# Kernel tuning notes

Measured on AMD Instinct MI355X. Metric: run time of the kernel, lower is better.

## Reference

```python
import jax, jax.numpy as jnp
import numpy as np

K = 10  # value-iteration steps


def _conv(x, w):
    # NCHW x OIHW -> NCHW, stride 1, SAME padding (pad=2 for 5x5, pad=0 for 1x1)
    return jax.lax.conv_general_dilated(
        x, w, window_strides=(1, 1), padding='SAME',
        dimension_numbers=('NCHW', 'OIHW', 'NCHW'))


def setup_inputs() -> dict:
    key = jax.random.key(0)
    ks = jax.random.split(key, 6)
    B, H, W = 64, 64, 64
    dim_h, n_hat, n_act = 150, 8, 4
    maze = jax.random.randint(ks[0], (B, H, W), 0, 3)
    # fixed embedding table from the torch module
    emb = jnp.array([[0.0, 0.0], [1.0, 0.0], [0.0, 10.0]], dtype=jnp.float32)
    encode_w = jax.random.normal(ks[1], (dim_h, 2, 5, 5), dtype=jnp.float32) * 0.05
    encode_b = jnp.zeros((dim_h,), dtype=jnp.float32)
    r_w = jax.random.normal(ks[2], (1, dim_h, 1, 1), dtype=jnp.float32) * 0.05
    q_w = jax.random.normal(ks[3], (n_hat, 1, 5, 5), dtype=jnp.float32) * 0.05
    # torch inits self.w to zeros; use small randn so the recurrence is non-trivial
    w = jax.random.normal(ks[4], (n_hat, 1, 5, 5), dtype=jnp.float32) * 0.05
    fc_w = jax.random.normal(ks[5], (n_act, n_hat), dtype=jnp.float32) * 0.1
    return dict(maze=maze, emb=emb, encode_w=encode_w, encode_b=encode_b,
                r_w=r_w, q_w=q_w, w=w, fc_w=fc_w)


def reference(maze, emb, encode_w, encode_b, r_w, q_w, w, fc_w):
    # embed: [B,H,W] -> [B,H,W,2] -> [B,2,H,W]
    m = emb[maze].transpose(0, 3, 1, 2)
    h = _conv(m, encode_w) + encode_b[None, :, None, None]  # [B,150,H,W]
    r = _conv(h, r_w)                                        # [B,1,H,W]
    q = _conv(r, q_w)                                        # [B,8,H,W]
    wk = jnp.concatenate([q_w, w], axis=1)                   # [8,2,5,5]

    def step(q, _):
        v = jnp.max(q, axis=1, keepdims=True)                # [B,1,H,W]
        q = _conv(jnp.concatenate([r, v], axis=1), wk)       # [B,8,H,W]
        return q, None

    q, _ = jax.lax.scan(step, q, None, length=K)
    q = q.transpose(0, 2, 3, 1)                              # [B,H,W,8]
    return q @ fc_w.T                                        # [B,H,W,4]
```

## Files before the change

kernel.cpp:

```cpp
#include <hip/hip_runtime.h>
#include <hip/hip_bf16.h>


#define NHAT 8
#define DIMH 150
#define VI_WAVES 12

typedef float v2f __attribute__((ext_vector_type(2)));

__global__ __launch_bounds__(512) void rq_kernel(
    const int* __restrict__ maze, const float* __restrict__ emb,
    const float* __restrict__ encode_w, const float* __restrict__ encode_b,
    const float* __restrict__ r_w, const float* __restrict__ q_w,
    float* __restrict__ q0g) {
  __shared__ float wpart[5][50];
  __shared__ float bpart[152];
  __shared__ float weff[2][25];
  __shared__ float Ts[4][25];
  __shared__ float bsh;
  __shared__ v2f qw2[25][4];
  __shared__ unsigned char mzt[24][68];
  __shared__ float rt[20][68];

  int tid = threadIdx.x;
  int b = blockIdx.y, A0 = blockIdx.x * 16;

  if (tid < 100) {
    int k = tid >> 2, j = tid & 3;
    qw2[k][j] = (v2f){q_w[(2 * j) * 25 + k], q_w[(2 * j + 1) * 25 + k]};
  }
  if (tid >= 256 && tid < 506) {
    int t2 = tid - 256;
    int chunk = t2 / 50, ik = t2 % 50;
    int i = ik / 25, k = ik % 25;
    int c0 = chunk * 30;
    float s = 0.f;
    for (int c = c0; c < c0 + 30; ++c)
      s += r_w[c] * encode_w[c * 50 + i * 25 + k];
    wpart[chunk][ik] = s;
  }
  if (tid >= 100 && tid < 250) {
    int c = tid - 100;
    bpart[c] = r_w[c] * encode_b[c];
  }
  for (int i = tid; i < 24 * 68; i += 512) {
    int mr = i / 68, mc = i % 68;
    int gy = A0 - 4 + mr, gx = mc - 2;
    unsigned char v = 3;
    if (gy >= 0 && gy < 64 && gx >= 0 && gx < 64)
      v = (unsigned char)maze[(b * 64 + gy) * 64 + gx];
    mzt[mr][mc] = v;
  }
  __syncthreads();
  if (tid < 50) {
    float s = 0.f;
#pragma unroll
    for (int ch = 0; ch < 5; ++ch) s += wpart[ch][tid];
    weff[tid / 25][tid % 25] = s;
  }
  if (tid == 50) {
    float s = 0.f;
    for (int c = 0; c < 150; ++c) s += bpart[c];
    bsh = s;
  }
  __syncthreads();
  if (tid < 100) {
    int val = tid / 25, k = tid % 25;
    float t = 0.f;
    if (val < 3) t = weff[0][k] * emb[val * 2] + weff[1][k] * emb[val * 2 + 1];
    Ts[val][k] = t;
  }
  __syncthreads();
  for (int i = tid; i < 20 * 68; i += 512) {
    int rr = i / 68, cc = i % 68;
    int gy = A0 - 2 + rr, gx = cc - 2;
    float v = 0.f;
    if (gy >= 0 && gy < 64 && gx >= 0 && gx < 64) {
      v = bsh;
#pragma unroll
      for (int ky = 0; ky < 5; ++ky)
#pragma unroll
        for (int kx = 0; kx < 5; ++kx)
          v += Ts[mzt[rr + ky][cc - 2 + kx]][ky * 5 + kx];
    }
    rt[rr][cc] = v;
  }
  __syncthreads();
  for (int i = tid; i < 16 * 64; i += 512) {
    int ly = i >> 6, gx = i & 63;
    int gy = A0 + ly;
    v2f acc[4];
#pragma unroll
    for (int j = 0; j < 4; ++j) acc[j] = (v2f){0.f, 0.f};
#pragma unroll
    for (int ky = 0; ky < 5; ++ky)
#pragma unroll
      for (int kx = 0; kx < 5; ++kx) {
        int k = ky * 5 + kx;
        float vv = rt[ly + ky][gx + kx];
        v2f vv2 = (v2f){vv, vv};
#pragma unroll
        for (int j = 0; j < 4; ++j) acc[j] += qw2[k][j] * vv2;
      }
#pragma unroll
    for (int j = 0; j < 4; ++j)
      *(v2f*)&q0g[(((size_t)(b * 64 + gy) * 4 + j) * 64 + gx) * 2] = acc[j];
  }
}

__global__ __launch_bounds__(768) void vi_kernel(
    const float* __restrict__ q0g, const float* __restrict__ w,
    const float* __restrict__ fc_w, float* __restrict__ out) {
  __shared__ __align__(16) float vbuf[2][60][68];
  __shared__ v2f wl2[25][4];

  int tid = threadIdx.x;
  int b = blockIdx.y, a0 = blockIdx.x * 16;
  int wave = tid >> 6, lane = tid & 63;
  int cq = lane >> 4;
  int p4 = (lane & 15) * 4;

  if (tid < 100) {
    int k = tid >> 2, j = tid & 3;
    wl2[k][j] = (v2f){w[(2 * j) * 25 + k], w[(2 * j + 1) * 25 + k]};
  }
  for (int i = tid; i < 2 * 60 * 68; i += 768) ((float*)vbuf)[i] = 0.f;
  __syncthreads();

  v2f wr[25];
#pragma unroll
  for (int k = 0; k < 25; ++k) wr[k] = wl2[k][cq];

  const float* q0b = q0g + (size_t)b * 64 * 4 * 64 * 2;
  int cur = 0;

  {
    int s = max(0, a0 - 20), e = min(64, a0 + 36);
    int gx = lane;
    for (int r = s + wave; r < e; r += VI_WAVES) {
      v2f a0v = *(const v2f*)&q0b[(((size_t)r * 4 + 0) * 64 + gx) * 2];
      v2f a1v = *(const v2f*)&q0b[(((size_t)r * 4 + 1) * 64 + gx) * 2];
      v2f a2v = *(const v2f*)&q0b[(((size_t)r * 4 + 2) * 64 + gx) * 2];
      v2f a3v = *(const v2f*)&q0b[(((size_t)r * 4 + 3) * 64 + gx) * 2];
      float m = fmaxf(fmaxf(fmaxf(a0v.x, a0v.y), fmaxf(a1v.x, a1v.y)),
                      fmaxf(fmaxf(a2v.x, a2v.y), fmaxf(a3v.x, a3v.y)));
      vbuf[0][r - a0 + 22][gx + 2] = m;
    }
  }
  __syncthreads();

  for (int t = 1; t <= 9; ++t) {
    int hh = 2 * (10 - t);
    int s = max(0, a0 - hh), e = min(64, a0 + 16 + hh);
    for (int r = s + wave; r < e; r += VI_WAVES) {
      int lr = r - a0 + 22;
      const float4* qp =
          (const float4*)&q0b[(((size_t)r * 4 + cq) * 64 + p4) * 2];
      float4 qv0 = qp[0], qv1 = qp[1];
      v2f aA[4];
#pragma unroll
      for (int j = 0; j < 4; ++j) aA[j] = (v2f){0.f, 0.f};
#pragma unroll
      for (int jj = 0; jj < 5; ++jj) {
        const float* row = &vbuf[cur][lr - 2 + jj][p4];
        float4 fa = *(const float4*)row;
        float4 fb = *(const float4*)(row + 4);
        float f[8] = {fa.x, fa.y, fa.z, fa.w, fb.x, fb.y, fb.z, fb.w};
#pragma unroll
        for (int kx = 0; kx < 5; ++kx) {
          v2f wk = wr[jj * 5 + kx];
#pragma unroll
          for (int j = 0; j < 4; ++j) {
            v2f vv2 = (v2f){f[j + kx], f[j + kx]};
            aA[j] += wk * vv2;
          }
        }
      }
      aA[0] += (v2f){qv0.x, qv0.y};
      aA[1] += (v2f){qv0.z, qv0.w};
      aA[2] += (v2f){qv1.x, qv1.y};
      aA[3] += (v2f){qv1.z, qv1.w};
      float m0 = fmaxf(aA[0].x, aA[0].y), m1 = fmaxf(aA[1].x, aA[1].y);
      float m2 = fmaxf(aA[2].x, aA[2].y), m3 = fmaxf(aA[3].x, aA[3].y);
      m0 = fmaxf(m0, __shfl_xor(m0, 16)); m0 = fmaxf(m0, __shfl_xor(m0, 32));
      m1 = fmaxf(m1, __shfl_xor(m1, 16)); m1 = fmaxf(m1, __shfl_xor(m1, 32));
      m2 = fmaxf(m2, __shfl_xor(m2, 16)); m2 = fmaxf(m2, __shfl_xor(m2, 32));
      m3 = fmaxf(m3, __shfl_xor(m3, 16)); m3 = fmaxf(m3, __shfl_xor(m3, 32));
      if (cq == 0) {
        *(v2f*)&vbuf[cur ^ 1][lr][2 + p4] = (v2f){m0, m1};
        *(v2f*)&vbuf[cur ^ 1][lr][4 + p4] = (v2f){m2, m3};
      }
    }
    __syncthreads();
    cur ^= 1;
  }

  for (int r = a0 + wave; r < a0 + 16; r += VI_WAVES) {
    int lr = r - a0 + 22;
    const float4* qp =
        (const float4*)&q0b[(((size_t)r * 4 + cq) * 64 + p4) * 2];
    float4 qv0 = qp[0], qv1 = qp[1];
    v2f aA[4];
#pragma unroll
    for (int j = 0; j < 4; ++j) aA[j] = (v2f){0.f, 0.f};
#pragma unroll
    for (int jj = 0; jj < 5; ++jj) {
      const float* row = &vbuf[cur][lr - 2 + jj][p4];
      float4 fa = *(const float4*)row;
      float4 fb = *(const float4*)(row + 4);
      float f[8] = {fa.x, fa.y, fa.z, fa.w, fb.x, fb.y, fb.z, fb.w};
#pragma unroll
      for (int kx = 0; kx < 5; ++kx) {
        v2f wk = wr[jj * 5 + kx];
#pragma unroll
        for (int j = 0; j < 4; ++j) {
          v2f vv2 = (v2f){f[j + kx], f[j + kx]};
          aA[j] += wk * vv2;
        }
      }
    }
    aA[0] += (v2f){qv0.x, qv0.y};
    aA[1] += (v2f){qv0.z, qv0.w};
    aA[2] += (v2f){qv1.x, qv1.y};
    aA[3] += (v2f){qv1.z, qv1.w};
    v2f fcp2[4];
#pragma unroll
    for (int a = 0; a < 4; ++a)
      fcp2[a] = (v2f){fc_w[a * 8 + 2 * cq], fc_w[a * 8 + 2 * cq + 1]};
#pragma unroll
    for (int j = 0; j < 4; ++j) {
      float p0 = fcp2[0].x * aA[j].x + fcp2[0].y * aA[j].y;
      float p1 = fcp2[1].x * aA[j].x + fcp2[1].y * aA[j].y;
      float p2 = fcp2[2].x * aA[j].x + fcp2[2].y * aA[j].y;
      float p3 = fcp2[3].x * aA[j].x + fcp2[3].y * aA[j].y;
      p0 += __shfl_xor(p0, 16); p0 += __shfl_xor(p0, 32);
      p1 += __shfl_xor(p1, 16); p1 += __shfl_xor(p1, 32);
      p2 += __shfl_xor(p2, 16); p2 += __shfl_xor(p2, 32);
      p3 += __shfl_xor(p3, 16); p3 += __shfl_xor(p3, 32);
      if (cq == 0)
        *(float4*)&out[((size_t)((b * 64 + r) * 64 + p4 + j)) * 4] =
            make_float4(p0, p1, p2, p3);
    }
  }
}

extern "C" void kernel_launch(void* const* d_in, const int* in_sizes, int n_in,
                              void* d_out, int out_size, void* d_ws, size_t ws_size,
                              hipStream_t stream) {
  const int* maze = (const int*)d_in[0];
  const float* emb = (const float*)d_in[1];
  const float* encode_w = (const float*)d_in[2];
  const float* encode_b = (const float*)d_in[3];
  const float* r_w = (const float*)d_in[4];
  const float* q_w = (const float*)d_in[5];
  const float* w = (const float*)d_in[6];
  const float* fc_w = (const float*)d_in[7];
  float* out = (float*)d_out;

  float* q0g = (float*)d_ws;

  rq_kernel<<<dim3(4, 64), 512, 0, stream>>>(maze, emb, encode_w, encode_b,
                                             r_w, q_w, q0g);
  vi_kernel<<<dim3(4, 64), 768, 0, stream>>>(q0g, w, fc_w, out);
}
```

Measured before the change: 113.9 us.

## Compute two output rows per wave in VI loop and use permlane swaps

Each wave in the value-iteration kernel now computes two adjacent rows per pass. It reads six shared-memory rows of v and reuses them for both rows' 5x5 stencils, where it used to read five rows per single output row. The cross-lane max and sum reductions switch from __shfl_xor to the permlane16/32 swap builtins when the compiler provides them, to avoid ds_bpermute traffic. In exchange, register pressure goes up, and fewer waves have work per pass on the trimmed halo ranges, so the load across waves can be less even.

```diff
diff --git a/kernel.cpp b/kernel.cpp
--- a/kernel.cpp
+++ b/kernel.cpp
@@ -7,6 +7,43 @@
 #define VI_WAVES 12
 
 typedef float v2f __attribute__((ext_vector_type(2)));
+
+__device__ __forceinline__ float xor16_max(float m) {
+#if __has_builtin(__builtin_amdgcn_permlane16_swap)
+  unsigned u = __float_as_uint(m);
+  auto r = __builtin_amdgcn_permlane16_swap(u, u, false, false);
+  return fmaxf(__uint_as_float(r[0]), __uint_as_float(r[1]));
+#else
+  return fmaxf(m, __shfl_xor(m, 16));
+#endif
+}
+__device__ __forceinline__ float xor32_max(float m) {
+#if __has_builtin(__builtin_amdgcn_permlane32_swap)
+  unsigned u = __float_as_uint(m);
+  auto r = __builtin_amdgcn_permlane32_swap(u, u, false, false);
+  return fmaxf(__uint_as_float(r[0]), __uint_as_float(r[1]));
+#else
+  return fmaxf(m, __shfl_xor(m, 32));
+#endif
+}
+__device__ __forceinline__ float xor16_add(float m) {
+#if __has_builtin(__builtin_amdgcn_permlane16_swap)
+  unsigned u = __float_as_uint(m);
+  auto r = __builtin_amdgcn_permlane16_swap(u, u, false, false);
+  return __uint_as_float(r[0]) + __uint_as_float(r[1]);
+#else
+  return m + __shfl_xor(m, 16);
+#endif
+}
+__device__ __forceinline__ float xor32_add(float m) {
+#if __has_builtin(__builtin_amdgcn_permlane32_swap)
+  unsigned u = __float_as_uint(m);
+  auto r = __builtin_amdgcn_permlane32_swap(u, u, false, false);
+  return __uint_as_float(r[0]) + __uint_as_float(r[1]);
+#else
+  return m + __shfl_xor(m, 32);
+#endif
+}
 
 __global__ __launch_bounds__(512) void rq_kernel(
     const int* __restrict__ maze, const float* __restrict__ emb,
@@ -152,93 +189,142 @@
   for (int t = 1; t <= 9; ++t) {
     int hh = 2 * (10 - t);
     int s = max(0, a0 - hh), e = min(64, a0 + 16 + hh);
-    for (int r = s + wave; r < e; r += VI_WAVES) {
-      int lr = r - a0 + 22;
-      const float4* qp =
-          (const float4*)&q0b[(((size_t)r * 4 + cq) * 64 + p4) * 2];
-      float4 qv0 = qp[0], qv1 = qp[1];
-      v2f aA[4];
-#pragma unroll
-      for (int j = 0; j < 4; ++j) aA[j] = (v2f){0.f, 0.f};
-#pragma unroll
-      for (int jj = 0; jj < 5; ++jj) {
+    for (int rb = s + 2 * wave; rb < e; rb += 2 * VI_WAVES) {
+      int lr = rb - a0 + 22;
+      const float4* qp0 =
+          (const float4*)&q0b[(((size_t)rb * 4 + cq) * 64 + p4) * 2];
+      const float4* qp1 =
+          (const float4*)&q0b[(((size_t)(rb + 1) * 4 + cq) * 64 + p4) * 2];
+      float4 q00 = qp0[0], q01 = qp0[1];
+      float4 q10 = qp1[0], q11 = qp1[1];
+      v2f A[4], Bv[4];
+#pragma unroll
+      for (int j = 0; j < 4; ++j) {
+        A[j] = (v2f){0.f, 0.f};
+        Bv[j] = (v2f){0.f, 0.f};
+      }
+#pragma unroll
+      for (int jj = 0; jj < 6; ++jj) {
         const float* row = &vbuf[cur][lr - 2 + jj][p4];
         float4 fa = *(const float4*)row;
         float4 fb = *(const float4*)(row + 4);
         float f[8] = {fa.x, fa.y, fa.z, fa.w, fb.x, fb.y, fb.z, fb.w};
-#pragma unroll
-        for (int kx = 0; kx < 5; ++kx) {
-          v2f wk = wr[jj * 5 + kx];
-#pragma unroll
-          for (int j = 0; j < 4; ++j) {
-            v2f vv2 = (v2f){f[j + kx], f[j + kx]};
-            aA[j] += wk * vv2;
+        if (jj < 5) {
+#pragma unroll
+          for (int kx = 0; kx < 5; ++kx) {
+            v2f wk = wr[jj * 5 + kx];
+#pragma unroll
+            for (int j = 0; j < 4; ++j)
+              A[j] += wk * (v2f){f[j + kx], f[j + kx]};
           }
         }
-      }
-      aA[0] += (v2f){qv0.x, qv0.y};
-      aA[1] += (v2f){qv0.z, qv0.w};
-      aA[2] += (v2f){qv1.x, qv1.y};
-      aA[3] += (v2f){qv1.z, qv1.w};
-      float m0 = fmaxf(aA[0].x, aA[0].y), m1 = fmaxf(aA[1].x, aA[1].y);
-      float m2 = fmaxf(aA[2].x, aA[2].y), m3 = fmaxf(aA[3].x, aA[3].y);
-      m0 = fmaxf(m0, __shfl_xor(m0, 16)); m0 = fmaxf(m0, __shfl_xor(m0, 32));
-      m1 = fmaxf(m1, __shfl_xor(m1, 16)); m1 = fmaxf(m1, __shfl_xor(m1, 32));
-      m2 = fmaxf(m2, __shfl_xor(m2, 16)); m2 = fmaxf(m2, __shfl_xor(m2, 32));
-      m3 = fmaxf(m3, __shfl_xor(m3, 16)); m3 = fmaxf(m3, __shfl_xor(m3, 32));
+        if (jj > 0) {
+#pragma unroll
+          for (int kx = 0; kx < 5; ++kx) {
+            v2f wk = wr[(jj - 1) * 5 + kx];
+#pragma unroll
+            for (int j = 0; j < 4; ++j)
+              Bv[j] += wk * (v2f){f[j + kx], f[j + kx]};
+          }
+        }
+      }
+      A[0] += (v2f){q00.x, q00.y};  A[1] += (v2f){q00.z, q00.w};
+      A[2] += (v2f){q01.x, q01.y};  A[3] += (v2f){q01.z, q01.w};
+      Bv[0] += (v2f){q10.x, q10.y}; Bv[1] += (v2f){q10.z, q10.w};
+      Bv[2] += (v2f){q11.x, q11.y}; Bv[3] += (v2f){q11.z, q11.w};
+      float m0 = fmaxf(A[0].x, A[0].y), m1 = fmaxf(A[1].x, A[1].y);
+      float m2 = fmaxf(A[2].x, A[2].y), m3 = fmaxf(A[3].x, A[3].y);
+      float n0 = fmaxf(Bv[0].x, Bv[0].y), n1 = fmaxf(Bv[1].x, Bv[1].y);
+      float n2 = fmaxf(Bv[2].x, Bv[2].y), n3 = fmaxf(Bv[3].x, Bv[3].y);
+      m0 = xor32_max(xor16_max(m0)); m1 = xor32_max(xor16_max(m1));
+      m2 = xor32_max(xor16_max(m2)); m3 = xor32_max(xor16_max(m3));
+      n0 = xor32_max(xor16_max(n0)); n1 = xor32_max(xor16_max(n1));
+      n2 = xor32_max(xor16_max(n2)); n3 = xor32_max(xor16_max(n3));
       if (cq == 0) {
         *(v2f*)&vbuf[cur ^ 1][lr][2 + p4] = (v2f){m0, m1};
         *(v2f*)&vbuf[cur ^ 1][lr][4 + p4] = (v2f){m2, m3};
+        *(v2f*)&vbuf[cur ^ 1][lr + 1][2 + p4] = (v2f){n0, n1};
+        *(v2f*)&vbuf[cur ^ 1][lr + 1][4 + p4] = (v2f){n2, n3};
       }
     }
     __syncthreads();
     cur ^= 1;
   }
 
-  for (int r = a0 + wave; r < a0 + 16; r += VI_WAVES) {
-    int lr = r - a0 + 22;
-    const float4* qp =
-        (const float4*)&q0b[(((size_t)r * 4 + cq) * 64 + p4) * 2];
-    float4 qv0 = qp[0], qv1 = qp[1];
-    v2f aA[4];
-#pragma unroll
-    for (int j = 0; j < 4; ++j) aA[j] = (v2f){0.f, 0.f};
-#pragma unroll
-    for (int jj = 0; jj < 5; ++jj) {
+  if (wave < 8) {
+    int rb = a0 + 2 * wave;
+    int lr = rb - a0 + 22;
+    const float4* qp0 =
+        (const float4*)&q0b[(((size_t)rb * 4 + cq) * 64 + p4) * 2];
+    const float4* qp1 =
+        (const float4*)&q0b[(((size_t)(rb + 1) * 4 + cq) * 64 + p4) * 2];
+    float4 q00 = qp0[0], q01 = qp0[1];
+    float4 q10 = qp1[0], q11 = qp1[1];
+    v2f A[4], Bv[4];
+#pragma unroll
+    for (int j = 0; j < 4; ++j) {
+      A[j] = (v2f){0.f, 0.f};
+      Bv[j] = (v2f){0.f, 0.f};
+    }
+#pragma unroll
+    for (int jj = 0; jj < 6; ++jj) {
       const float* row = &vbuf[cur][lr - 2 + jj][p4];
       float4 fa = *(const float4*)row;
       float4 fb = *(const float4*)(row + 4);
       float f[8] = {fa.x, fa.y, fa.z, fa.w, fb.x, fb.y, fb.z, fb.w};
-#pragma unroll
-      for (int kx = 0; kx < 5; ++kx) {
-        v2f wk = wr[jj * 5 + kx];
-#pragma unroll
-        for (int j = 0; j < 4; ++j) {
-          v2f vv2 = (v2f){f[j + kx], f[j + kx]};
-          aA[j] += wk * vv2;
+      if (jj < 5) {
+#pragma unroll
+        for (int kx = 0; kx < 5; ++kx) {
+          v2f wk = wr[jj * 5 + kx];
+#pragma unroll
+          for (int j = 0; j < 4; ++j)
+            A[j] += wk * (v2f){f[j + kx], f[j + kx]};
         }
       }
-    }
-    aA[0] += (v2f){qv0.x, qv0.y};
-    aA[1] += (v2f){qv0.z, qv0.w};
-    aA[2] += (v2f){qv1.x, qv1.y};
-    aA[3] += (v2f){qv1.z, qv1.w};
+      if (jj > 0) {
+#pragma unroll
+        for (int kx = 0; kx < 5; ++kx) {
+          v2f wk = wr[(jj - 1) * 5 + kx];
+#pragma unroll
+          for (int j = 0; j < 4; ++j)
+            Bv[j] += wk * (v2f){f[j + kx], f[j + kx]};
+        }
+      }
+    }
+    A[0] += (v2f){q00.x, q00.y};  A[1] += (v2f){q00.z, q00.w};
+    A[2] += (v2f){q01.x, q01.y};  A[3] += (v2f){q01.z, q01.w};
+    Bv[0] += (v2f){q10.x, q10.y}; Bv[1] += (v2f){q10.z, q10.w};
+    Bv[2] += (v2f){q11.x, q11.y}; Bv[3] += (v2f){q11.z, q11.w};
     v2f fcp2[4];
 #pragma unroll
     for (int a = 0; a < 4; ++a)
       fcp2[a] = (v2f){fc_w[a * 8 + 2 * cq], fc_w[a * 8 + 2 * cq + 1]};
 #pragma unroll
     for (int j = 0; j < 4; ++j) {
-      float p0 = fcp2[0].x * aA[j].x + fcp2[0].y * aA[j].y;
-      float p1 = fcp2[1].x * aA[j].x + fcp2[1].y * aA[j].y;
-      float p2 = fcp2[2].x * aA[j].x + fcp2[2].y * aA[j].y;
-      float p3 = fcp2[3].x * aA[j].x + fcp2[3].y * aA[j].y;
-      p0 += __shfl_xor(p0, 16); p0 += __shfl_xor(p0, 32);
-      p1 += __shfl_xor(p1, 16); p1 += __shfl_xor(p1, 32);
-      p2 += __shfl_xor(p2, 16); p2 += __shfl_xor(p2, 32);
-      p3 += __shfl_xor(p3, 16); p3 += __shfl_xor(p3, 32);
+      float p0 = fcp2[0].x * A[j].x + fcp2[0].y * A[j].y;
+      float p1 = fcp2[1].x * A[j].x + fcp2[1].y * A[j].y;
+      float p2 = fcp2[2].x * A[j].x + fcp2[2].y * A[j].y;
+      float p3 = fcp2[3].x * A[j].x + fcp2[3].y * A[j].y;
+      p0 = xor32_add(xor16_add(p0));
+      p1 = xor32_add(xor16_add(p1));
+      p2 = xor32_add(xor16_add(p2));
+      p3 = xor32_add(xor16_add(p3));
       if (cq == 0)
-        *(float4*)&out[((size_t)((b * 64 + r) * 64 + p4 + j)) * 4] =
+        *(float4*)&out[((size_t)((b * 64 + rb) * 64 + p4 + j)) * 4] =
+            make_float4(p0, p1, p2, p3);
+    }
+#pragma unroll
+    for (int j = 0; j < 4; ++j) {
+      float p0 = fcp2[0].x * Bv[j].x + fcp2[0].y * Bv[j].y;
+      float p1 = fcp2[1].x * Bv[j].x + fcp2[1].y * Bv[j].y;
+      float p2 = fcp2[2].x * Bv[j].x + fcp2[2].y * Bv[j].y;
+      float p3 = fcp2[3].x * Bv[j].x + fcp2[3].y * Bv[j].y;
+      p0 = xor32_add(xor16_add(p0));
+      p1 = xor32_add(xor16_add(p1));
+      p2 = xor32_add(xor16_add(p2));
+      p3 = xor32_add(xor16_add(p3));
+      if (cq == 0)
+        *(float4*)&out[((size_t)((b * 64 + rb + 1) * 64 + p4 + j)) * 4] =
             make_float4(p0, p1, p2, p3);
     }
   }
```

Measured after the change: 115.3 us. No clear change (+1.2%).
